# Performance work log

Measured on AMD Instinct MI355X. Metric: run time of the kernel, lower is better.

## Reference

```python
import jax, jax.numpy as jnp
import numpy as np

N_NODES = 50000
N_EDGES = 800000
IN_DIM = 128
HIDDEN = 128
CLASSES = 64


def setup_inputs() -> dict:
    key = jax.random.key(0)
    ks = jax.random.split(key, 10)
    features = jax.random.normal(ks[0], (N_NODES, IN_DIM), dtype=jnp.float32)
    W1 = jax.random.normal(ks[1], (HIDDEN, IN_DIM), dtype=jnp.float32) * (2.0 / np.sqrt(IN_DIM + HIDDEN))
    b1 = jnp.zeros((HIDDEN,), dtype=jnp.float32)
    W2 = jax.random.normal(ks[2], (CLASSES, HIDDEN), dtype=jnp.float32) * (2.0 / np.sqrt(HIDDEN + CLASSES))
    b2 = jnp.zeros((CLASSES,), dtype=jnp.float32)
    order_attn = jax.random.uniform(ks[3], (2,), dtype=jnp.float32)
    src1 = jax.random.randint(ks[4], (N_EDGES,), 0, N_NODES, dtype=jnp.int32)
    dst1 = jax.random.randint(ks[5], (N_EDGES,), 0, N_NODES, dtype=jnp.int32)
    src2 = jax.random.randint(ks[6], (N_EDGES,), 0, N_NODES, dtype=jnp.int32)
    dst2 = jax.random.randint(ks[7], (N_EDGES,), 0, N_NODES, dtype=jnp.int32)
    return {"features": features, "W1": W1, "b1": b1, "W2": W2, "b2": b2,
            "order_attn": order_attn, "src1": src1, "dst1": dst1,
            "src2": src2, "dst2": dst2}


def _gin_conv(x, src, dst, W, b):
    # DGL GINConv, aggregator_type='sum', eps=0 (default, non-learnable):
    # h_v = Linear( x_v + sum_{(u->v) in E} x_u )
    agg = jax.ops.segment_sum(x[src], dst, num_segments=N_NODES)  # [N, D]
    return (x + agg) @ W.T + b


def reference(features, W1, b1, W2, b2, order_attn, src1, dst1, src2, dst2):
    a0, a1 = order_attn[0], order_attn[1]
    # layer 1 over both order-graphs
    x11 = jax.nn.elu(a0 * _gin_conv(features, src1, dst1, W1, b1))
    x12 = jax.nn.elu(a1 * _gin_conv(features, src2, dst2, W1, b1))
    x1 = x11 + x12  # [N, hidden]
    # layer 2 over both order-graphs
    x21 = jax.nn.elu(a0 * _gin_conv(x1, src1, dst1, W2, b2))
    x22 = jax.nn.elu(a1 * _gin_conv(x1, src2, dst2, W2, b2))
    return x21 + x22  # [N, classes]
```

## Files before the change

### kernel.cpp

```cpp
#include <hip/hip_runtime.h>
#include <math.h>

#define N_NODES 50000
#define N_EDGES 800000
#define IN_DIM 128
#define HIDDEN 128
#define CLASSES 64
#define N2 100000

#define BIN_SHIFT 8
#define BIN_SZ 256
#define NB 391
#define NBLK 256
#define CHUNK ((2 * N_EDGES + NBLK - 1) / NBLK)

static __device__ __forceinline__ float elu_f(float x) {
    return x > 0.f ? x : (expf(x) - 1.f);
}

static __device__ __forceinline__ void fma4(float4& a, const float4 w, const float s) {
    a.x = fmaf(w.x, s, a.x);
    a.y = fmaf(w.y, s, a.y);
    a.z = fmaf(w.z, s, a.z);
    a.w = fmaf(w.w, s, a.w);
}

static __device__ __forceinline__ unsigned pack_bf2(float a, float b) {
    unsigned ua = __float_as_uint(a);
    ua = (ua + 0x7FFFu + ((ua >> 16) & 1u)) >> 16;
    unsigned ub = __float_as_uint(b);
    ub = (ub + 0x7FFFu + ((ub >> 16) & 1u)) >> 16;
    return ua | (ub << 16);
}

static __device__ __forceinline__ float2 bf2f2(unsigned u) {
    float2 r;
    r.x = __uint_as_float(u << 16);
    r.y = __uint_as_float(u & 0xFFFF0000u);
    return r;
}

__global__ __launch_bounds__(1024) void k_p1_count(
    const int* __restrict__ dst1, const int* __restrict__ dst2,
    int* __restrict__ counts)
{
    __shared__ int hist[NB];
    const int t = threadIdx.x, b = blockIdx.x;
    if (t < NB) hist[t] = 0;
    __syncthreads();
    const int beg = b * CHUNK;
    const int end = min(beg + CHUNK, 2 * N_EDGES);
    for (int i = beg + t; i < end; i += 1024) {
        const int idx = (i < N_EDGES) ? dst1[i] : (N_NODES + dst2[i - N_EDGES]);
        atomicAdd(&hist[idx >> BIN_SHIFT], 1);
    }
    __syncthreads();
    if (t < NB) counts[t * NBLK + b] = hist[t];
}

__global__ __launch_bounds__(512) void k_scan_bins(
    int* __restrict__ counts, int* __restrict__ binStart, int* __restrict__ off)
{
    __shared__ int tot[512];
    const int t = threadIdx.x;
    int total = 0;
    if (t < NB) {
        const int4* p = reinterpret_cast<const int4*>(counts + t * NBLK);
        #pragma unroll 8
        for (int i = 0; i < NBLK / 4; ++i) {
            const int4 c = p[i];
            total += (c.x + c.y) + (c.z + c.w);
        }
    }
    tot[t] = (t < NB) ? total : 0;
    __syncthreads();
    const int v = tot[t];
    for (int d = 1; d < 512; d <<= 1) {
        const int x = (t >= d) ? tot[t - d] : 0;
        __syncthreads();
        tot[t] += x;
        __syncthreads();
    }
    const int excl = tot[t] - v;
    if (t < NB) binStart[t] = excl;
    if (t == NB - 1) binStart[NB] = tot[t];
    if (t == 0) off[N2] = 2 * N_EDGES;
    if (t < NB) {
        int run = excl;
        int* p = counts + t * NBLK;
        for (int i = 0; i < NBLK; i += 4) {
            int4 c = *reinterpret_cast<int4*>(p + i);
            int4 w;
            w.x = run; run += c.x;
            w.y = run; run += c.y;
            w.z = run; run += c.z;
            w.w = run; run += c.w;
            *reinterpret_cast<int4*>(p + i) = w;
        }
    }
}

__global__ __launch_bounds__(1024) void k_p2_scatter(
    const int* __restrict__ src1, const int* __restrict__ dst1,
    const int* __restrict__ src2, const int* __restrict__ dst2,
    const int* __restrict__ counts, unsigned* __restrict__ binned)
{
    __shared__ int cur[NB];
    const int t = threadIdx.x, b = blockIdx.x;
    if (t < NB) cur[t] = counts[t * NBLK + b];
    __syncthreads();
    const int beg = b * CHUNK;
    const int end = min(beg + CHUNK, 2 * N_EDGES);
    for (int i = beg + t; i < end; i += 1024) {
        int s, idx;
        if (i < N_EDGES) { s = src1[i]; idx = dst1[i]; }
        else             { s = src2[i - N_EDGES]; idx = N_NODES + dst2[i - N_EDGES]; }
        const int bin = idx >> BIN_SHIFT;
        const unsigned rec = ((unsigned)s << BIN_SHIFT) | (unsigned)(idx & (BIN_SZ - 1));
        const int pos = atomicAdd(&cur[bin], 1);
        binned[pos] = rec;
    }
}

__global__ __launch_bounds__(1024) void k_p3_csr(
    const unsigned* __restrict__ binned, const int* __restrict__ binStart,
    int* __restrict__ off, int* __restrict__ csr)
{
    __shared__ int hist[BIN_SZ], sc[BIN_SZ], cur[BIN_SZ];
    const int t = threadIdx.x, bin = blockIdx.x;
    const int bs = binStart[bin], be = binStart[bin + 1];
    const int base = bin << BIN_SHIFT;
    const int nloc = min(BIN_SZ, N2 - base);
    if (t < BIN_SZ) hist[t] = 0;
    __syncthreads();
    for (int p = bs + t; p < be; p += 1024)
        atomicAdd(&hist[binned[p] & (BIN_SZ - 1u)], 1);
    __syncthreads();
    int v = 0;
    if (t < BIN_SZ) { v = hist[t]; sc[t] = v; }
    __syncthreads();
    for (int d = 1; d < BIN_SZ; d <<= 1) {
        int x = 0;
        if (t < BIN_SZ && t >= d) x = sc[t - d];
        __syncthreads();
        if (t < BIN_SZ) sc[t] += x;
        __syncthreads();
    }
    if (t < BIN_SZ) {
        const int excl = sc[t] - v;
        cur[t] = bs + excl;
        if (t < nloc) off[base + t] = bs + excl;
    }
    __syncthreads();
    for (int p = bs + t; p < be; p += 1024) {
        const unsigned rec = binned[p];
        const int pos = atomicAdd(&cur[rec & (BIN_SZ - 1u)], 1);
        csr[pos] = (int)(rec >> BIN_SHIFT);
    }
}

__global__ __launch_bounds__(256) void k_gemm1(
    const float* __restrict__ f, const float* __restrict__ W1,
    unsigned short* __restrict__ y1b)
{
    __shared__ float Wt[IN_DIM][HIDDEN + 4];
    __shared__ float S[16][IN_DIM];

    const int t = threadIdx.x;
    for (int i = t; i < HIDDEN * IN_DIM; i += 256) {
        const int o = i >> 7, k = i & 127;
        Wt[k][o] = W1[i];
    }
    const int o4 = (t & 31) * 4;
    const int ln = t >> 5;

    const int ntiles = N_NODES / 16;
    for (int tile = blockIdx.x; tile < ntiles; tile += gridDim.x) {
        const int v0 = tile * 16;
        __syncthreads();
        for (int i = t; i < 16 * IN_DIM; i += 256) {
            const int r = i >> 7, k = i & 127;
            S[r][k] = f[(size_t)(v0 + r) * IN_DIM + k];
        }
        __syncthreads();

        float4 acc1 = {0.f, 0.f, 0.f, 0.f};
        float4 acc2 = {0.f, 0.f, 0.f, 0.f};
        const float* s1 = S[ln * 2];
        const float* s2 = S[ln * 2 + 1];
        #pragma unroll 8
        for (int k = 0; k < IN_DIM; k += 4) {
            const float4 sa = *reinterpret_cast<const float4*>(s1 + k);
            const float4 sb = *reinterpret_cast<const float4*>(s2 + k);
            const float4 w0 = *reinterpret_cast<const float4*>(&Wt[k + 0][o4]);
            const float4 w1 = *reinterpret_cast<const float4*>(&Wt[k + 1][o4]);
            const float4 w2 = *reinterpret_cast<const float4*>(&Wt[k + 2][o4]);
            const float4 w3 = *reinterpret_cast<const float4*>(&Wt[k + 3][o4]);
            fma4(acc1, w0, sa.x); fma4(acc1, w1, sa.y); fma4(acc1, w2, sa.z); fma4(acc1, w3, sa.w);
            fma4(acc2, w0, sb.x); fma4(acc2, w1, sb.y); fma4(acc2, w2, sb.z); fma4(acc2, w3, sb.w);
        }
        const int na = v0 + ln * 2, nb = na + 1;
        uint2 pa, pb;
        pa.x = pack_bf2(acc1.x, acc1.y); pa.y = pack_bf2(acc1.z, acc1.w);
        pb.x = pack_bf2(acc2.x, acc2.y); pb.y = pack_bf2(acc2.z, acc2.w);
        *reinterpret_cast<uint2*>(y1b + (size_t)na * HIDDEN + o4) = pa;
        *reinterpret_cast<uint2*>(y1b + (size_t)nb * HIDDEN + o4) = pb;
    }
}

__global__ __launch_bounds__(256) void k_gemm2(
    const float* __restrict__ x1, const float* __restrict__ W2,
    unsigned short* __restrict__ y2b)
{
    __shared__ float Wt[IN_DIM][CLASSES + 4];
    __shared__ float S[32][IN_DIM];

    const int t = threadIdx.x;
    for (int i = t; i < CLASSES * IN_DIM; i += 256) {
        const int c = i >> 7, k = i & 127;
        Wt[k][c] = W2[i];
    }
    const int c4 = (t & 15) * 4;
    const int ln = t >> 4;

    const int ntiles = (N_NODES + 31) / 32;
    for (int tile = blockIdx.x; tile < ntiles; tile += gridDim.x) {
        const int v0 = tile * 32;
        __syncthreads();
        for (int i = t; i < 32 * IN_DIM; i += 256) {
            const int r = i >> 7, k = i & 127;
            const int node = v0 + r;
            S[r][k] = (node < N_NODES) ? x1[(size_t)node * IN_DIM + k] : 0.f;
        }
        __syncthreads();

        float4 acc1 = {0.f, 0.f, 0.f, 0.f};
        float4 acc2 = {0.f, 0.f, 0.f, 0.f};
        const float* s1 = S[ln * 2];
        const float* s2 = S[ln * 2 + 1];
        #pragma unroll 8
        for (int k = 0; k < IN_DIM; k += 4) {
            const float4 sa = *reinterpret_cast<const float4*>(s1 + k);
            const float4 sb = *reinterpret_cast<const float4*>(s2 + k);
            const float4 w0 = *reinterpret_cast<const float4*>(&Wt[k + 0][c4]);
            const float4 w1 = *reinterpret_cast<const float4*>(&Wt[k + 1][c4]);
            const float4 w2 = *reinterpret_cast<const float4*>(&Wt[k + 2][c4]);
            const float4 w3 = *reinterpret_cast<const float4*>(&Wt[k + 3][c4]);
            fma4(acc1, w0, sa.x); fma4(acc1, w1, sa.y); fma4(acc1, w2, sa.z); fma4(acc1, w3, sa.w);
            fma4(acc2, w0, sb.x); fma4(acc2, w1, sb.y); fma4(acc2, w2, sb.z); fma4(acc2, w3, sb.w);
        }
        const int na = v0 + ln * 2, nb = na + 1;
        uint2 pa, pb;
        pa.x = pack_bf2(acc1.x, acc1.y); pa.y = pack_bf2(acc1.z, acc1.w);
        pb.x = pack_bf2(acc2.x, acc2.y); pb.y = pack_bf2(acc2.z, acc2.w);
        if (na < N_NODES) *reinterpret_cast<uint2*>(y2b + (size_t)na * CLASSES + c4) = pa;
        if (nb < N_NODES) *reinterpret_cast<uint2*>(y2b + (size_t)nb * CLASSES + c4) = pb;
    }
}

__global__ __launch_bounds__(256) void k_pull1(
    const unsigned short* __restrict__ y1b,
    const int* __restrict__ off, const int* __restrict__ csr,
    const float* __restrict__ b1, const float* __restrict__ attn,
    float* __restrict__ x1)
{
    const int lane = threadIdx.x & 63;
    const int v = (blockIdx.x * 256 + threadIdx.x) >> 6;
    if (v >= N_NODES) return;
    const int c = lane * 2;

    float2 acc1 = {0.f, 0.f}, acc2 = {0.f, 0.f};
    #pragma unroll
    for (int g = 0; g < 2; ++g) {
        const int idx = g * N_NODES + v;
        const int beg = off[idx], end_ = off[idx + 1];
        float2 acc = {0.f, 0.f};
        for (int j = beg; j < end_; j += 8) {
            #pragma unroll
            for (int u = 0; u < 8; ++u) {
                const int jj = j + u;
                const int s = csr[min(jj, end_ - 1)];
                const float2 r = bf2f2(*reinterpret_cast<const unsigned*>(
                    y1b + (size_t)s * HIDDEN + c));
                const float m = (jj < end_) ? 1.f : 0.f;
                acc.x = fmaf(m, r.x, acc.x);
                acc.y = fmaf(m, r.y, acc.y);
            }
        }
        if (g == 0) acc1 = acc; else acc2 = acc;
    }

    const float2 yv = bf2f2(*reinterpret_cast<const unsigned*>(y1b + (size_t)v * HIDDEN + c));
    const float2 bb = *reinterpret_cast<const float2*>(b1 + c);
    const float a0 = attn[0], a1 = attn[1];
    float2 r;
    r.x = elu_f(a0 * (yv.x + acc1.x + bb.x)) + elu_f(a1 * (yv.x + acc2.x + bb.x));
    r.y = elu_f(a0 * (yv.y + acc1.y + bb.y)) + elu_f(a1 * (yv.y + acc2.y + bb.y));
    *reinterpret_cast<float2*>(x1 + (size_t)v * HIDDEN + c) = r;
}

__global__ __launch_bounds__(256) void k_pull2(
    const unsigned short* __restrict__ y2b,
    const int* __restrict__ off, const int* __restrict__ csr,
    const float* __restrict__ b2, const float* __restrict__ attn,
    float* __restrict__ out)
{
    const int lane = threadIdx.x & 63;
    const int v = (blockIdx.x * 256 + threadIdx.x) >> 6;
    if (v >= N_NODES) return;
    const int half = lane >> 5;
    const int l = lane & 31;
    const int c = l * 2;

    const int idx = half * N_NODES + v;
    const int beg = off[idx], end_ = off[idx + 1];
    float2 acc = {0.f, 0.f};
    for (int j = beg; j < end_; j += 8) {
        #pragma unroll
        for (int u = 0; u < 8; ++u) {
            const int jj = j + u;
            const int s = csr[min(jj, end_ - 1)];
            const float2 r = bf2f2(*reinterpret_cast<const unsigned*>(
                y2b + (size_t)s * CLASSES + c));
            const float m = (jj < end_) ? 1.f : 0.f;
            acc.x = fmaf(m, r.x, acc.x);
            acc.y = fmaf(m, r.y, acc.y);
        }
    }

    float2 other;
    other.x = __shfl(acc.x, lane ^ 32);
    other.y = __shfl(acc.y, lane ^ 32);
    const float2 g1 = (half == 0) ? acc : other;
    const float2 g2 = (half == 0) ? other : acc;

    const float2 yv = bf2f2(*reinterpret_cast<const unsigned*>(y2b + (size_t)v * CLASSES + c));
    const float2 bb = *reinterpret_cast<const float2*>(b2 + c);
    const float a0 = attn[0], a1 = attn[1];
    float2 r;
    r.x = elu_f(a0 * (yv.x + g1.x + bb.x)) + elu_f(a1 * (yv.x + g2.x + bb.x));
    r.y = elu_f(a0 * (yv.y + g1.y + bb.y)) + elu_f(a1 * (yv.y + g2.y + bb.y));
    if (half == 0)
        *reinterpret_cast<float2*>(out + (size_t)v * CLASSES + c) = r;
}

extern "C" void kernel_launch(void* const* d_in, const int* in_sizes, int n_in,
                              void* d_out, int out_size, void* d_ws, size_t ws_size,
                              hipStream_t stream)
{
    const float* features = (const float*)d_in[0];
    const float* W1   = (const float*)d_in[1];
    const float* b1   = (const float*)d_in[2];
    const float* W2   = (const float*)d_in[3];
    const float* b2   = (const float*)d_in[4];
    const float* attn = (const float*)d_in[5];
    const int* src1   = (const int*)d_in[6];
    const int* dst1   = (const int*)d_in[7];
    const int* src2   = (const int*)d_in[8];
    const int* dst2   = (const int*)d_in[9];
    float* out = (float*)d_out;

    float* x1 = (float*)d_ws;
    unsigned short* y1b = (unsigned short*)(x1 + (size_t)N_NODES * HIDDEN);
    unsigned short* y2b = y1b + (size_t)N_NODES * HIDDEN;
    int* off      = (int*)(y2b + (size_t)N_NODES * CLASSES);
    int* binStart = off + (N2 + 4);
    int* counts   = binStart + 392;
    unsigned* binned = (unsigned*)(counts + NB * NBLK);
    int* csr      = (int*)(binned + 2 * N_EDGES);

    k_p1_count  <<<NBLK, 1024, 0, stream>>>(dst1, dst2, counts);
    k_scan_bins <<<1, 512, 0, stream>>>(counts, binStart, off);
    k_p2_scatter<<<NBLK, 1024, 0, stream>>>(src1, dst1, src2, dst2, counts, binned);
    k_p3_csr    <<<NB, 1024, 0, stream>>>(binned, binStart, off, csr);

    k_gemm1<<<1024, 256, 0, stream>>>(features, W1, y1b);
    k_pull1<<<12500, 256, 0, stream>>>(y1b, off, csr, b1, attn, x1);

    k_gemm2<<<782, 256, 0, stream>>>(x1, W2, y2b);
    k_pull2<<<12500, 256, 0, stream>>>(y2b, off, csr, b2, attn, out);
}
```

Baseline: 329.8 us.

## Split edges across half-waves with 8-byte gathers in pull kernels

```diff
diff --git a/kernel.cpp b/kernel.cpp
--- a/kernel.cpp
+++ b/kernel.cpp
@@ -38,6 +38,12 @@
     r.x = __uint_as_float(u << 16);
     r.y = __uint_as_float(u & 0xFFFF0000u);
     return r;
+}
+
+static __device__ __forceinline__ void acc4(float4& a, const uint2 u) {
+    const float2 lo = bf2f2(u.x);
+    const float2 hi = bf2f2(u.y);
+    a.x += lo.x; a.y += lo.y; a.z += hi.x; a.w += hi.y;
 }
 
 __global__ __launch_bounds__(1024) void k_p1_count(
@@ -267,36 +273,58 @@
     const int lane = threadIdx.x & 63;
     const int v = (blockIdx.x * 256 + threadIdx.x) >> 6;
     if (v >= N_NODES) return;
-    const int c = lane * 2;
-
-    float2 acc1 = {0.f, 0.f}, acc2 = {0.f, 0.f};
+    const int half = lane >> 5;
+    const int l = lane & 31;
+    const int c4 = l * 4;
+
+    float4 tot1, tot2;
     #pragma unroll
     for (int g = 0; g < 2; ++g) {
         const int idx = g * N_NODES + v;
         const int beg = off[idx], end_ = off[idx + 1];
-        float2 acc = {0.f, 0.f};
-        for (int j = beg; j < end_; j += 8) {
-            #pragma unroll
-            for (int u = 0; u < 8; ++u) {
-                const int jj = j + u;
-                const int s = csr[min(jj, end_ - 1)];
-                const float2 r = bf2f2(*reinterpret_cast<const unsigned*>(
-                    y1b + (size_t)s * HIDDEN + c));
-                const float m = (jj < end_) ? 1.f : 0.f;
-                acc.x = fmaf(m, r.x, acc.x);
-                acc.y = fmaf(m, r.y, acc.y);
-            }
-        }
-        if (g == 0) acc1 = acc; else acc2 = acc;
-    }
-
-    const float2 yv = bf2f2(*reinterpret_cast<const unsigned*>(y1b + (size_t)v * HIDDEN + c));
-    const float2 bb = *reinterpret_cast<const float2*>(b1 + c);
-    const float a0 = attn[0], a1 = attn[1];
-    float2 r;
-    r.x = elu_f(a0 * (yv.x + acc1.x + bb.x)) + elu_f(a1 * (yv.x + acc2.x + bb.x));
-    r.y = elu_f(a0 * (yv.y + acc1.y + bb.y)) + elu_f(a1 * (yv.y + acc2.y + bb.y));
-    *reinterpret_cast<float2*>(x1 + (size_t)v * HIDDEN + c) = r;
+        float4 acc = {0.f, 0.f, 0.f, 0.f};
+        int j = beg;
+        for (; j + 8 <= end_; j += 8) {
+            const int s0 = csr[j + half];
+            const int s1 = csr[j + 2 + half];
+            const int s2 = csr[j + 4 + half];
+            const int s3 = csr[j + 6 + half];
+            const uint2 u0 = *reinterpret_cast<const uint2*>(y1b + ((s0 << 7) + c4));
+            const uint2 u1 = *reinterpret_cast<const uint2*>(y1b + ((s1 << 7) + c4));
+            const uint2 u2 = *reinterpret_cast<const uint2*>(y1b + ((s2 << 7) + c4));
+            const uint2 u3 = *reinterpret_cast<const uint2*>(y1b + ((s3 << 7) + c4));
+            acc4(acc, u0); acc4(acc, u1); acc4(acc, u2); acc4(acc, u3);
+        }
+        for (; j + 2 <= end_; j += 2) {
+            const int s = csr[j + half];
+            const uint2 u = *reinterpret_cast<const uint2*>(y1b + ((s << 7) + c4));
+            acc4(acc, u);
+        }
+        if (j < end_ && half == 0) {
+            const int s = csr[j];
+            const uint2 u = *reinterpret_cast<const uint2*>(y1b + ((s << 7) + c4));
+            acc4(acc, u);
+        }
+        float4 t;
+        t.x = acc.x + __shfl_xor(acc.x, 32);
+        t.y = acc.y + __shfl_xor(acc.y, 32);
+        t.z = acc.z + __shfl_xor(acc.z, 32);
+        t.w = acc.w + __shfl_xor(acc.w, 32);
+        if (g == 0) tot1 = t; else tot2 = t;
+    }
+
+    if (half == 0) {
+        const uint2 uy = *reinterpret_cast<const uint2*>(y1b + ((v << 7) + c4));
+        const float2 ylo = bf2f2(uy.x), yhi = bf2f2(uy.y);
+        const float4 bb = *reinterpret_cast<const float4*>(b1 + c4);
+        const float a0 = attn[0], a1 = attn[1];
+        float4 r;
+        r.x = elu_f(a0 * (ylo.x + tot1.x + bb.x)) + elu_f(a1 * (ylo.x + tot2.x + bb.x));
+        r.y = elu_f(a0 * (ylo.y + tot1.y + bb.y)) + elu_f(a1 * (ylo.y + tot2.y + bb.y));
+        r.z = elu_f(a0 * (yhi.x + tot1.z + bb.z)) + elu_f(a1 * (yhi.x + tot2.z + bb.z));
+        r.w = elu_f(a0 * (yhi.y + tot1.w + bb.w)) + elu_f(a1 * (yhi.y + tot2.w + bb.w));
+        *reinterpret_cast<float4*>(x1 + (size_t)v * HIDDEN + c4) = r;
+    }
 }
 
 __global__ __launch_bounds__(256) void k_pull2(
@@ -308,40 +336,61 @@
     const int lane = threadIdx.x & 63;
     const int v = (blockIdx.x * 256 + threadIdx.x) >> 6;
     if (v >= N_NODES) return;
-    const int half = lane >> 5;
-    const int l = lane & 31;
-    const int c = l * 2;
-
-    const int idx = half * N_NODES + v;
+    const int g_sel = lane >> 5;
+    const int par = (lane >> 4) & 1;
+    const int l = lane & 15;
+    const int c4 = l * 4;
+
+    const int idx = g_sel * N_NODES + v;
     const int beg = off[idx], end_ = off[idx + 1];
-    float2 acc = {0.f, 0.f};
-    for (int j = beg; j < end_; j += 8) {
-        #pragma unroll
-        for (int u = 0; u < 8; ++u) {
-            const int jj = j + u;
-            const int s = csr[min(jj, end_ - 1)];
-            const float2 r = bf2f2(*reinterpret_cast<const unsigned*>(
-                y2b + (size_t)s * CLASSES + c));
-            const float m = (jj < end_) ? 1.f : 0.f;
-            acc.x = fmaf(m, r.x, acc.x);
-            acc.y = fmaf(m, r.y, acc.y);
-        }
-    }
-
-    float2 other;
-    other.x = __shfl(acc.x, lane ^ 32);
-    other.y = __shfl(acc.y, lane ^ 32);
-    const float2 g1 = (half == 0) ? acc : other;
-    const float2 g2 = (half == 0) ? other : acc;
-
-    const float2 yv = bf2f2(*reinterpret_cast<const unsigned*>(y2b + (size_t)v * CLASSES + c));
-    const float2 bb = *reinterpret_cast<const float2*>(b2 + c);
-    const float a0 = attn[0], a1 = attn[1];
-    float2 r;
-    r.x = elu_f(a0 * (yv.x + g1.x + bb.x)) + elu_f(a1 * (yv.x + g2.x + bb.x));
-    r.y = elu_f(a0 * (yv.y + g1.y + bb.y)) + elu_f(a1 * (yv.y + g2.y + bb.y));
-    if (half == 0)
-        *reinterpret_cast<float2*>(out + (size_t)v * CLASSES + c) = r;
+    float4 acc = {0.f, 0.f, 0.f, 0.f};
+    int j = beg;
+    for (; j + 8 <= end_; j += 8) {
+        const int s0 = csr[j + par];
+        const int s1 = csr[j + 2 + par];
+        const int s2 = csr[j + 4 + par];
+        const int s3 = csr[j + 6 + par];
+        const uint2 u0 = *reinterpret_cast<const uint2*>(y2b + ((s0 << 6) + c4));
+        const uint2 u1 = *reinterpret_cast<const uint2*>(y2b + ((s1 << 6) + c4));
+        const uint2 u2 = *reinterpret_cast<const uint2*>(y2b + ((s2 << 6) + c4));
+        const uint2 u3 = *reinterpret_cast<const uint2*>(y2b + ((s3 << 6) + c4));
+        acc4(acc, u0); acc4(acc, u1); acc4(acc, u2); acc4(acc, u3);
+    }
+    for (; j + 2 <= end_; j += 2) {
+        const int s = csr[j + par];
+        const uint2 u = *reinterpret_cast<const uint2*>(y2b + ((s << 6) + c4));
+        acc4(acc, u);
+    }
+    if (j < end_ && par == 0) {
+        const int s = csr[j];
+        const uint2 u = *reinterpret_cast<const uint2*>(y2b + ((s << 6) + c4));
+        acc4(acc, u);
+    }
+
+    acc.x += __shfl_xor(acc.x, 16);
+    acc.y += __shfl_xor(acc.y, 16);
+    acc.z += __shfl_xor(acc.z, 16);
+    acc.w += __shfl_xor(acc.w, 16);
+    float4 other;
+    other.x = __shfl_xor(acc.x, 32);
+    other.y = __shfl_xor(acc.y, 32);
+    other.z = __shfl_xor(acc.z, 32);
+    other.w = __shfl_xor(acc.w, 32);
+    const float4 t1 = (g_sel == 0) ? acc : other;
+    const float4 t2 = (g_sel == 0) ? other : acc;
+
+    if (lane < 16) {
+        const uint2 uy = *reinterpret_cast<const uint2*>(y2b + ((v << 6) + c4));
+        const float2 ylo = bf2f2(uy.x), yhi = bf2f2(uy.y);
+        const float4 bb = *reinterpret_cast<const float4*>(b2 + c4);
+        const float a0 = attn[0], a1 = attn[1];
+        float4 r;
+        r.x = elu_f(a0 * (ylo.x + t1.x + bb.x)) + elu_f(a1 * (ylo.x + t2.x + bb.x));
+        r.y = elu_f(a0 * (ylo.y + t1.y + bb.y)) + elu_f(a1 * (ylo.y + t2.y + bb.y));
+        r.z = elu_f(a0 * (yhi.x + t1.z + bb.z)) + elu_f(a1 * (yhi.x + t2.z + bb.z));
+        r.w = elu_f(a0 * (yhi.y + t1.w + bb.w)) + elu_f(a1 * (yhi.y + t2.w + bb.w));
+        *reinterpret_cast<float4*>(out + (size_t)v * CLASSES + c4) = r;
+    }
 }
 
 extern "C" void kernel_launch(void* const* d_in, const int* in_sizes, int n_in,
@@ -374,9 +423,9 @@
     k_p2_scatter<<<NBLK, 1024, 0, stream>>>(src1, dst1, src2, dst2, counts, binned);
     k_p3_csr    <<<NB, 1024, 0, stream>>>(binned, binStart, off, csr);
 
-    k_gemm1<<<1024, 256, 0, stream>>>(features, W1, y1b);
+    k_gemm1<<<3125, 256, 0, stream>>>(features, W1, y1b);
     k_pull1<<<12500, 256, 0, stream>>>(y1b, off, csr, b1, attn, x1);
 
-    k_gemm2<<<782, 256, 0, stream>>>(x1, W2, y2b);
+    k_gemm2<<<1563, 256, 0, stream>>>(x1, W2, y2b);
     k_pull2<<<12500, 256, 0, stream>>>(y2b, off, csr, b2, attn, out);
 }
```

Result: slower. 345.7 us (+4.8%).
